# Kernel tuning notes

Measured on AMD Instinct MI355X. Metric: run time of the kernel, lower is better.

The kernel has to match this reference:

```python
import jax, jax.numpy as jnp
import numpy as np
import math

D_MODEL = 1024
N_HEADS = 16
D_K = D_MODEL // N_HEADS
SEQ_LEN = 2048
BATCH = 2


def setup_inputs() -> dict:
    key = jax.random.key(0)
    ks = jax.random.split(key, 5)
    X = jax.random.normal(ks[0], (BATCH, SEQ_LEN, D_MODEL), dtype=jnp.float32)
    # Linear params (torch Linear: y = x @ W.T + b). Store as [in, out] for einsum.
    sc1 = 1.0 / math.sqrt(D_MODEL)
    W_qkv = jax.random.uniform(ks[1], (D_MODEL, 3 * D_MODEL), jnp.float32, -sc1, sc1)
    b_qkv = jax.random.uniform(ks[2], (3 * D_MODEL,), jnp.float32, -sc1, sc1)
    W_out = jax.random.uniform(ks[3], (D_MODEL, D_MODEL), jnp.float32, -sc1, sc1)
    b_out = jax.random.uniform(ks[4], (D_MODEL,), jnp.float32, -sc1, sc1)
    return {"X": X, "W_qkv": W_qkv, "b_qkv": b_qkv, "W_out": W_out, "b_out": b_out}


def reference(X, W_qkv, b_qkv, W_out, b_out):
    B, S, E = X.shape
    qkv = X @ W_qkv + b_qkv                       # [B,S,3E]
    qkv = qkv.reshape(B, S, 3, N_HEADS, D_K)
    q = jnp.transpose(qkv[:, :, 0], (0, 2, 1, 3))  # [B,H,S,Dk]
    k = jnp.transpose(qkv[:, :, 1], (0, 2, 1, 3))
    v = jnp.transpose(qkv[:, :, 2], (0, 2, 1, 3))
    scores = jnp.einsum('bhqd,bhkd->bhqk', q, k) / math.sqrt(D_K)
    causal = jnp.tril(jnp.ones((S, S), dtype=bool))
    scores = jnp.where(causal[None, None], scores, -jnp.inf)
    probs = jax.nn.softmax(scores, axis=-1)
    out = jnp.einsum('bhqk,bhkd->bhqd', probs, v)  # [B,H,S,Dk]
    out = jnp.transpose(out, (0, 2, 1, 3)).reshape(B, S, E)
    return out @ W_out + b_out
```

## Files before the change

### kernel.cpp

```cpp
#include <hip/hip_runtime.h>

typedef __bf16 bf16_t;
typedef bf16_t bf16x8 __attribute__((ext_vector_type(8)));
typedef bf16_t bf16x4 __attribute__((ext_vector_type(4)));
typedef float f32x4 __attribute__((ext_vector_type(4)));

#define SEQLEN 2048
#define EMB 1024
#define NHEADS 16
#define N3 3072
#define NBATCH 2
#define NEG_INF (-__builtin_inff())
#define SC2 0.18033688011112042f

__device__ __forceinline__ void async16(bf16_t* lds, const bf16_t* g) {
    __builtin_amdgcn_global_load_lds(
        (const __attribute__((address_space(1))) void*)g,
        (__attribute__((address_space(3))) void*)lds, 16, 0, 0);
}

__global__ __launch_bounds__(256) void prep_kernel(
    const float* __restrict__ X, const float* __restrict__ Wqkv,
    const float* __restrict__ Wout, bf16_t* __restrict__ Xb,
    bf16_t* __restrict__ Wqkv_t, bf16_t* __restrict__ Wout_t)
{
    __shared__ float tile[64][65];
    const int id = blockIdx.x;
    const int t = threadIdx.x;
    if (id < 2048) {
        const int i = (id * 256 + t) * 8;
        float4 a = *(const float4*)&X[i];
        float4 b = *(const float4*)&X[i + 4];
        bf16_t v[8];
        v[0] = (bf16_t)a.x; v[1] = (bf16_t)a.y; v[2] = (bf16_t)a.z; v[3] = (bf16_t)a.w;
        v[4] = (bf16_t)b.x; v[5] = (bf16_t)b.y; v[6] = (bf16_t)b.z; v[7] = (bf16_t)b.w;
        *(float4*)&Xb[i] = *(float4*)&v[0];
        return;
    }
    const int wid2 = id - 2048;
    int bx = wid2 & 63;
    const int k0 = (wid2 >> 6) << 6;
    const float* W; bf16_t* Wt; int N; float s;
    if (bx < 48) { W = Wqkv; Wt = Wqkv_t; N = N3;  s = (bx * 64 < EMB) ? SC2 : 1.0f; }
    else         { bx -= 48; W = Wout; Wt = Wout_t; N = EMB; s = 1.0f; }
    const int n0 = bx * 64;
    const int nl = t & 63, k4 = t >> 6;
#pragma unroll
    for (int i = 0; i < 16; ++i) {
        int kk = k4 + i * 4;
        tile[kk][nl] = W[(size_t)(k0 + kk) * N + n0 + nl];
    }
    __syncthreads();
    const int kl = t & 63, n4 = t >> 6;
#pragma unroll
    for (int i = 0; i < 16; ++i) {
        int nn = n4 + i * 4;
        Wt[(size_t)(n0 + nn) * EMB + k0 + kl] = (bf16_t)(tile[kl][nn] * s);
    }
}

template<bool OUT_BF16, bool V_SPLIT>
__global__ __launch_bounds__(256) void gemm_bt_kernel(
    const bf16_t* __restrict__ A, const bf16_t* __restrict__ Bt,
    const float* __restrict__ bias, void* __restrict__ Cp,
    bf16_t* __restrict__ vt, int scale_q,
    int Mdim, int Ndim, int Kdim)
{
    __shared__ bf16_t As[128 * 64];
    __shared__ bf16_t Bs[128 * 64];
    const int nb = Ndim >> 7;
    const int cpx = gridDim.x >> 3;
    const int bid = (blockIdx.x & 7) * cpx + (blockIdx.x >> 3);
    const int bx = bid % nb, by = bid / nb;
    const int r0 = by << 7, c0 = bx << 7;
    const int t = threadIdx.x, lane = t & 63;
    const int wid = t >> 6;
    const int wm = wid >> 1, wn = wid & 1;
    const int lr = lane & 15, lg = lane >> 4;

    const int glrow = wid * 32 + (lane >> 3);
    const int gsw = ((lane & 7) ^ (lane >> 3)) << 3;
    const bf16_t* gA = &A[(size_t)(r0 + glrow) * Kdim + gsw];
    const bf16_t* gB = &Bt[(size_t)(c0 + glrow) * Kdim + gsw];
    bf16_t* ldsA = &As[wid * 2048];
    bf16_t* ldsB = &Bs[wid * 2048];
    const size_t row8 = (size_t)8 * Kdim;

    const int fragb0 = (lr * 128 + lg * 16) ^ ((lr & 7) << 4);
    const int fragb1 = (lr * 128 + 64 + lg * 16) ^ ((lr & 7) << 4);

    f32x4 acc[4][4] = {};
    const int KT = Kdim >> 6;
    for (int kt = 0; kt < KT; ++kt) {
        const bf16_t* a = gA + kt * 64;
        const bf16_t* b = gB + kt * 64;
        async16(ldsA,        a);
        async16(ldsA + 512,  a + row8);
        async16(ldsA + 1024, a + 2 * row8);
        async16(ldsA + 1536, a + 3 * row8);
        async16(ldsB,        b);
        async16(ldsB + 512,  b + row8);
        async16(ldsB + 1024, b + 2 * row8);
        async16(ldsB + 1536, b + 3 * row8);
        __syncthreads();

        const char* Ab = (const char*)As + wm * 8192;
        const char* Bb = (const char*)Bs + wn * 8192;
        bf16x8 af[4], bfm[4];
#pragma unroll
        for (int m = 0; m < 4; ++m)
            af[m] = *(const bf16x8*)(Ab + m * 2048 + fragb0);
#pragma unroll
        for (int n = 0; n < 4; ++n)
            bfm[n] = *(const bf16x8*)(Bb + n * 2048 + fragb0);
#pragma unroll
        for (int m = 0; m < 4; ++m)
#pragma unroll
            for (int n = 0; n < 4; ++n)
                acc[m][n] = __builtin_amdgcn_mfma_f32_16x16x32_bf16(
                    af[m], bfm[n], acc[m][n], 0, 0, 0);
#pragma unroll
        for (int m = 0; m < 4; ++m)
            af[m] = *(const bf16x8*)(Ab + m * 2048 + fragb1);
#pragma unroll
        for (int n = 0; n < 4; ++n)
            bfm[n] = *(const bf16x8*)(Bb + n * 2048 + fragb1);
#pragma unroll
        for (int m = 0; m < 4; ++m)
#pragma unroll
            for (int n = 0; n < 4; ++n)
                acc[m][n] = __builtin_amdgcn_mfma_f32_16x16x32_bf16(
                    af[m], bfm[n], acc[m][n], 0, 0, 0);
        __syncthreads();
    }

    const bool vmode = V_SPLIT && (c0 >= 2 * EMB);
    const int lgp = ((lg & 1) << 1) | (lg >> 1);
#pragma unroll
    for (int m = 0; m < 4; ++m) {
#pragma unroll
        for (int n = 0; n < 4; ++n) {
            const int col = c0 + wn * 64 + n * 16 + lr;
            float bval = bias[col];
            if (scale_q && col < EMB) bval *= SC2;
            if (vmode) {
                const int h = (col - 2 * EMB) >> 6, dd = col & 63;
                const int bb = r0 >> 11;
                const int sbase = (r0 & (SEQLEN - 1)) + wm * 64 + m * 16 + lgp * 4;
                bf16x4 pk;
#pragma unroll
                for (int j = 0; j < 4; ++j) pk[j] = (bf16_t)(acc[m][n][j] + bval);
                *(bf16x4*)&vt[(size_t)((bb * 16 + h) * 64 + dd) * SEQLEN + sbase] = pk;
            } else {
#pragma unroll
                for (int j = 0; j < 4; ++j) {
                    const int row = r0 + wm * 64 + m * 16 + lg * 4 + j;
                    const float v = acc[m][n][j] + bval;
                    if (OUT_BF16)
                        ((bf16_t*)Cp)[(size_t)row * Ndim + col] = (bf16_t)v;
                    else
                        ((float*)Cp)[(size_t)row * Ndim + col] = v;
                }
            }
        }
    }
}

__global__ __launch_bounds__(256, 4) void attn_kernel(
    const bf16_t* __restrict__ qkv, const bf16_t* __restrict__ vt,
    bf16_t* __restrict__ attn_out)
{
    __shared__ bf16_t Kl[2][4096];
    __shared__ bf16_t Vl[2][4096];
    const int d = blockIdx.x;
    const int r = d >> 8;
    const int u = (d >> 3) & 31;
    int qt = (r & 1) ? (31 - u) : u;
    if (r & 2) qt ^= 16;
    const int bh = (d & 7) + (r << 3);
    const int b = bh >> 4, h = bh & 15;
    const int q0 = qt << 6;
    const int t = threadIdx.x, lane = t & 63, wid = t >> 6;
    const int lr = lane & 15, lg = lane >> 4;
    const int sr = t >> 2, sc16 = (t & 3) << 4;

    const int fragb0 = (lr * 128 + lg * 16) ^ ((lr & 7) << 4);
    const int fragb1 = (lr * 128 + 64 + lg * 16) ^ ((lr & 7) << 4);
    const int stb0   = (sr * 128 + sc16 * 2) ^ ((sr & 7) << 4);
    const int stb1   = (sr * 128 + sc16 * 2 + 16) ^ ((sr & 7) << 4);

    const bf16_t* kp = &qkv[(size_t)(b * SEQLEN + sr) * N3 + EMB + h * 64 + sc16];
    const bf16_t* vp = &vt[(size_t)(bh * 64 + sr) * SEQLEN + sc16];
    const size_t kstep = (size_t)64 * N3;

    const int qg = q0 + wid * 16 + lr;
    bf16x8 qa0, qa1;
    {
        const bf16_t* qb = &qkv[(size_t)(b * SEQLEN + qg) * N3 + h * 64];
        qa0 = *(const bf16x8*)&qb[lg * 8];
        qa1 = *(const bf16x8*)&qb[32 + lg * 8];
    }
    bf16x8 ones;
#pragma unroll
    for (int i = 0; i < 8; ++i) ones[i] = (bf16_t)1.0f;

    f32x4 o[4] = {};
    f32x4 ol = {};
    float m_run = NEG_INF;

    auto stT = [&](char* base, float4 a, float4 c) {
        *(float4*)(base + stb0) = a; *(float4*)(base + stb1) = c;
    };

    {
        float4 k0 = *(const float4*)kp, k1 = *(const float4*)(kp + 8);
        float4 v0 = *(const float4*)vp, v1 = *(const float4*)(vp + 8);
        stT((char*)Kl[0], k0, k1);
        stT((char*)Vl[0], v0, v1);
    }
    __syncthreads();
    int cur = 0;
    for (int kt = 0; kt <= qt; ++kt) {
        float4 nk0, nk1, nv0, nv1;
        const bool more = (kt < qt);
        if (more) {
            kp += kstep; vp += 64;
            nk0 = *(const float4*)kp; nk1 = *(const float4*)(kp + 8);
            nv0 = *(const float4*)vp; nv1 = *(const float4*)(vp + 8);
        }

        const char* Kc = (const char*)Kl[cur];
        const char* Vc = (const char*)Vl[cur];

        f32x4 sc[4] = {};
        __builtin_amdgcn_s_setprio(1);
#pragma unroll
        for (int n = 0; n < 4; ++n) {
            bf16x8 kb0 = *(const bf16x8*)(Kc + (fragb0 + n * 2048));
            bf16x8 kb1 = *(const bf16x8*)(Kc + (fragb1 + n * 2048));
            sc[n] = __builtin_amdgcn_mfma_f32_16x16x32_bf16(kb0, qa0, sc[n], 0, 0, 0);
            sc[n] = __builtin_amdgcn_mfma_f32_16x16x32_bf16(kb1, qa1, sc[n], 0, 0, 0);
        }
        __builtin_amdgcn_s_setprio(0);

        if (kt == qt) {
#pragma unroll
            for (int n = 0; n < 4; ++n)
#pragma unroll
                for (int j = 0; j < 4; ++j) {
                    const int kg = kt * 64 + n * 16 + lg * 4 + j;
                    sc[n][j] = (kg <= qg) ? sc[n][j] : NEG_INF;
                }
        }
        float mx[4];
#pragma unroll
        for (int n = 0; n < 4; ++n)
            mx[n] = fmaxf(fmaxf(fmaxf(sc[n][0], sc[n][1]), sc[n][2]), sc[n][3]);
        float pmax = fmaxf(fmaxf(fmaxf(mx[0], mx[1]), mx[2]), mx[3]);

        if (__any(pmax > m_run + 8.f)) {
            float pm = fmaxf(pmax, __shfl_xor(pmax, 16));
            pm = fmaxf(pm, __shfl_xor(pm, 32));
            const float mnew = fmaxf(m_run, pm);
            const float alpha = exp2f(m_run - mnew);
            m_run = mnew;
            float al[4];
#pragma unroll
            for (int j = 0; j < 4; ++j) al[j] = __shfl(alpha, lg * 4 + j);
#pragma unroll
            for (int dn = 0; dn < 4; ++dn)
#pragma unroll
                for (int j = 0; j < 4; ++j) o[dn][j] *= al[j];
#pragma unroll
            for (int j = 0; j < 4; ++j) ol[j] *= al[j];
        }

#pragma unroll
        for (int n = 0; n < 4; ++n)
#pragma unroll
            for (int j = 0; j < 4; ++j) sc[n][j] = exp2f(sc[n][j] - m_run);

        unsigned pk00, pk01, pk10, pk11, pk20, pk21, pk30, pk31;
        asm("v_cvt_pk_bf16_f32 %0, %1, %2" : "=v"(pk00) : "v"(sc[0][0]), "v"(sc[0][1]));
        asm("v_cvt_pk_bf16_f32 %0, %1, %2" : "=v"(pk01) : "v"(sc[0][2]), "v"(sc[0][3]));
        asm("v_cvt_pk_bf16_f32 %0, %1, %2" : "=v"(pk10) : "v"(sc[1][0]), "v"(sc[1][1]));
        asm("v_cvt_pk_bf16_f32 %0, %1, %2" : "=v"(pk11) : "v"(sc[1][2]), "v"(sc[1][3]));
        asm("v_cvt_pk_bf16_f32 %0, %1, %2" : "=v"(pk20) : "v"(sc[2][0]), "v"(sc[2][1]));
        asm("v_cvt_pk_bf16_f32 %0, %1, %2" : "=v"(pk21) : "v"(sc[2][2]), "v"(sc[2][3]));
        asm("v_cvt_pk_bf16_f32 %0, %1, %2" : "=v"(pk30) : "v"(sc[3][0]), "v"(sc[3][1]));
        asm("v_cvt_pk_bf16_f32 %0, %1, %2" : "=v"(pk31) : "v"(sc[3][2]), "v"(sc[3][3]));
        asm("v_permlane32_swap_b32 %0, %1" : "+v"(pk00), "+v"(pk10));
        asm("v_permlane32_swap_b32 %0, %1" : "+v"(pk01), "+v"(pk11));
        asm("v_permlane32_swap_b32 %0, %1" : "+v"(pk20), "+v"(pk30));
        asm("v_permlane32_swap_b32 %0, %1" : "+v"(pk21), "+v"(pk31));
        union UW { unsigned w[4]; bf16x8 v; };
        UW ua, ub;
        ua.w[0] = pk00; ua.w[1] = pk01; ua.w[2] = pk10; ua.w[3] = pk11;
        ub.w[0] = pk20; ub.w[1] = pk21; ub.w[2] = pk30; ub.w[3] = pk31;
        const bf16x8 pa0 = ua.v, pa1 = ub.v;

        __builtin_amdgcn_s_setprio(1);
#pragma unroll
        for (int dn = 0; dn < 4; ++dn) {
            bf16x8 vb0 = *(const bf16x8*)(Vc + (fragb0 + dn * 2048));
            bf16x8 vb1 = *(const bf16x8*)(Vc + (fragb1 + dn * 2048));
            o[dn] = __builtin_amdgcn_mfma_f32_16x16x32_bf16(pa0, vb0, o[dn], 0, 0, 0);
            o[dn] = __builtin_amdgcn_mfma_f32_16x16x32_bf16(pa1, vb1, o[dn], 0, 0, 0);
        }
        ol = __builtin_amdgcn_mfma_f32_16x16x32_bf16(pa0, ones, ol, 0, 0, 0);
        ol = __builtin_amdgcn_mfma_f32_16x16x32_bf16(pa1, ones, ol, 0, 0, 0);
        __builtin_amdgcn_s_setprio(0);

        if (more) {
            stT((char*)Kl[cur ^ 1], nk0, nk1);
            stT((char*)Vl[cur ^ 1], nv0, nv1);
        }
        __syncthreads();
        cur ^= 1;
    }

    float li[4];
#pragma unroll
    for (int j = 0; j < 4; ++j) li[j] = 1.0f / ol[j];
#pragma unroll
    for (int dn = 0; dn < 4; ++dn)
#pragma unroll
        for (int j = 0; j < 4; ++j) {
            const int row = b * SEQLEN + q0 + wid * 16 + lg * 4 + j;
            attn_out[(size_t)row * EMB + h * 64 + dn * 16 + lr] =
                (bf16_t)(o[dn][j] * li[j]);
        }
}

extern "C" void kernel_launch(void* const* d_in, const int* in_sizes, int n_in,
                              void* d_out, int out_size, void* d_ws, size_t ws_size,
                              hipStream_t stream)
{
    const float* X     = (const float*)d_in[0];
    const float* W_qkv = (const float*)d_in[1];
    const float* b_qkv = (const float*)d_in[2];
    const float* W_out = (const float*)d_in[3];
    const float* b_out = (const float*)d_in[4];
    float* out = (float*)d_out;

    char* ws = (char*)d_ws;
    bf16_t* Wqkv_t = (bf16_t*)ws;
    bf16_t* Wout_t = (bf16_t*)(ws + 6u * 1024 * 1024);
    bf16_t* qkv    = (bf16_t*)(ws + 8u * 1024 * 1024);
    bf16_t* attn   = (bf16_t*)(ws + 32u * 1024 * 1024);
    bf16_t* Xb     = (bf16_t*)(ws + 40u * 1024 * 1024);
    bf16_t* Vt_g   = (bf16_t*)(ws + 48u * 1024 * 1024);

    dim3 blk(256);
    prep_kernel<<<3072, blk, 0, stream>>>(X, W_qkv, W_out, Xb, Wqkv_t, Wout_t);

    gemm_bt_kernel<true, true><<<(4096 / 128) * (N3 / 128), blk, 0, stream>>>(
        Xb, Wqkv_t, b_qkv, (void*)qkv, Vt_g, 1, 4096, N3, EMB);

    attn_kernel<<<32 * 32, blk, 0, stream>>>(qkv, Vt_g, attn);

    gemm_bt_kernel<false, false><<<(4096 / 128) * (EMB / 128), blk, 0, stream>>>(
        attn, Wout_t, b_out, (void*)out, nullptr, 0, 4096, EMB, EMB);
}
```

Before: 108.3 us.

## Use 128-row query tiles with 8 waves sharing each K/V tile in attention

The attention kernel now launches 512 blocks of 512 threads, each covering 128 query rows, so eight waves share one staged K/V tile instead of four. Each thread loads one 16-byte chunk per tile, and waves whose queries lie entirely before a key tile skip its compute while still joining the barrier. The block-to-tile mapping is changed to pair long and short causal tiles. This halves K/V global loads and LDS staging per query, at the cost of idle waves on diagonal tiles and fewer, larger blocks.

```diff
diff --git a/kernel.cpp b/kernel.cpp
--- a/kernel.cpp
+++ b/kernel.cpp
@@ -166,7 +166,7 @@
     }
 }
 
-__global__ __launch_bounds__(256, 4) void attn_kernel(
+__global__ __launch_bounds__(512, 4) void attn_kernel(
     const bf16_t* __restrict__ qkv, const bf16_t* __restrict__ vt,
     bf16_t* __restrict__ attn_out)
 {
@@ -174,31 +174,31 @@
     __shared__ bf16_t Vl[2][4096];
     const int d = blockIdx.x;
     const int r = d >> 8;
-    const int u = (d >> 3) & 31;
-    int qt = (r & 1) ? (31 - u) : u;
-    if (r & 2) qt ^= 16;
-    const int bh = (d & 7) + (r << 3);
+    const int u = (d >> 5) & 7;
+    const int bh = d & 31;
+    const int qt = r ? u : (15 - u);
     const int b = bh >> 4, h = bh & 15;
-    const int q0 = qt << 6;
+    const int q0 = qt << 7;
+    const int ktend = 2 * qt + 1;
     const int t = threadIdx.x, lane = t & 63, wid = t >> 6;
     const int lr = lane & 15, lg = lane >> 4;
-    const int sr = t >> 2, sc16 = (t & 3) << 4;
+    const int sr = t >> 3, sc8 = (t & 7) << 3;
 
     const int fragb0 = (lr * 128 + lg * 16) ^ ((lr & 7) << 4);
     const int fragb1 = (lr * 128 + 64 + lg * 16) ^ ((lr & 7) << 4);
-    const int stb0   = (sr * 128 + sc16 * 2) ^ ((sr & 7) << 4);
-    const int stb1   = (sr * 128 + sc16 * 2 + 16) ^ ((sr & 7) << 4);
-
-    const bf16_t* kp = &qkv[(size_t)(b * SEQLEN + sr) * N3 + EMB + h * 64 + sc16];
-    const bf16_t* vp = &vt[(size_t)(bh * 64 + sr) * SEQLEN + sc16];
+    const int stb    = (sr * 128 + sc8 * 2) ^ ((sr & 7) << 4);
+
+    const bf16_t* kp = &qkv[(size_t)(b * SEQLEN + sr) * N3 + EMB + h * 64 + sc8];
+    const bf16_t* vp = &vt[(size_t)(bh * 64 + sr) * SEQLEN + sc8];
     const size_t kstep = (size_t)64 * N3;
 
-    const int qg = q0 + wid * 16 + lr;
+    const int qb = q0 + wid * 16;
+    const int qg = qb + lr;
     bf16x8 qa0, qa1;
     {
-        const bf16_t* qb = &qkv[(size_t)(b * SEQLEN + qg) * N3 + h * 64];
-        qa0 = *(const bf16x8*)&qb[lg * 8];
-        qa1 = *(const bf16x8*)&qb[32 + lg * 8];
+        const bf16_t* qp = &qkv[(size_t)(b * SEQLEN + qg) * N3 + h * 64];
+        qa0 = *(const bf16x8*)&qp[lg * 8];
+        qa1 = *(const bf16x8*)&qp[32 + lg * 8];
     }
     bf16x8 ones;
 #pragma unroll
@@ -208,112 +208,111 @@
     f32x4 ol = {};
     float m_run = NEG_INF;
 
-    auto stT = [&](char* base, float4 a, float4 c) {
-        *(float4*)(base + stb0) = a; *(float4*)(base + stb1) = c;
-    };
-
     {
-        float4 k0 = *(const float4*)kp, k1 = *(const float4*)(kp + 8);
-        float4 v0 = *(const float4*)vp, v1 = *(const float4*)(vp + 8);
-        stT((char*)Kl[0], k0, k1);
-        stT((char*)Vl[0], v0, v1);
+        float4 k0 = *(const float4*)kp;
+        float4 v0 = *(const float4*)vp;
+        *(float4*)((char*)Kl[0] + stb) = k0;
+        *(float4*)((char*)Vl[0] + stb) = v0;
     }
     __syncthreads();
     int cur = 0;
-    for (int kt = 0; kt <= qt; ++kt) {
-        float4 nk0, nk1, nv0, nv1;
-        const bool more = (kt < qt);
+    for (int kt = 0; kt <= ktend; ++kt) {
+        float4 nk, nv;
+        const bool more = (kt < ktend);
         if (more) {
             kp += kstep; vp += 64;
-            nk0 = *(const float4*)kp; nk1 = *(const float4*)(kp + 8);
-            nv0 = *(const float4*)vp; nv1 = *(const float4*)(vp + 8);
-        }
-
-        const char* Kc = (const char*)Kl[cur];
-        const char* Vc = (const char*)Vl[cur];
-
-        f32x4 sc[4] = {};
-        __builtin_amdgcn_s_setprio(1);
-#pragma unroll
-        for (int n = 0; n < 4; ++n) {
-            bf16x8 kb0 = *(const bf16x8*)(Kc + (fragb0 + n * 2048));
-            bf16x8 kb1 = *(const bf16x8*)(Kc + (fragb1 + n * 2048));
-            sc[n] = __builtin_amdgcn_mfma_f32_16x16x32_bf16(kb0, qa0, sc[n], 0, 0, 0);
-            sc[n] = __builtin_amdgcn_mfma_f32_16x16x32_bf16(kb1, qa1, sc[n], 0, 0, 0);
-        }
-        __builtin_amdgcn_s_setprio(0);
-
-        if (kt == qt) {
+            nk = *(const float4*)kp;
+            nv = *(const float4*)vp;
+        }
+
+        const int kbase = kt << 6;
+        if (kbase <= qb + 15) {
+            const char* Kc = (const char*)Kl[cur];
+            const char* Vc = (const char*)Vl[cur];
+
+            f32x4 sc[4] = {};
+            __builtin_amdgcn_s_setprio(1);
+#pragma unroll
+            for (int n = 0; n < 4; ++n) {
+                bf16x8 kb0 = *(const bf16x8*)(Kc + (fragb0 + n * 2048));
+                bf16x8 kb1 = *(const bf16x8*)(Kc + (fragb1 + n * 2048));
+                sc[n] = __builtin_amdgcn_mfma_f32_16x16x32_bf16(kb0, qa0, sc[n], 0, 0, 0);
+                sc[n] = __builtin_amdgcn_mfma_f32_16x16x32_bf16(kb1, qa1, sc[n], 0, 0, 0);
+            }
+            __builtin_amdgcn_s_setprio(0);
+
+            if (kbase + 63 > qb) {
+#pragma unroll
+                for (int n = 0; n < 4; ++n)
+#pragma unroll
+                    for (int j = 0; j < 4; ++j) {
+                        const int kg = kbase + n * 16 + lg * 4 + j;
+                        sc[n][j] = (kg <= qg) ? sc[n][j] : NEG_INF;
+                    }
+            }
+            float mx[4];
 #pragma unroll
             for (int n = 0; n < 4; ++n)
-#pragma unroll
-                for (int j = 0; j < 4; ++j) {
-                    const int kg = kt * 64 + n * 16 + lg * 4 + j;
-                    sc[n][j] = (kg <= qg) ? sc[n][j] : NEG_INF;
-                }
-        }
-        float mx[4];
-#pragma unroll
-        for (int n = 0; n < 4; ++n)
-            mx[n] = fmaxf(fmaxf(fmaxf(sc[n][0], sc[n][1]), sc[n][2]), sc[n][3]);
-        float pmax = fmaxf(fmaxf(fmaxf(mx[0], mx[1]), mx[2]), mx[3]);
-
-        if (__any(pmax > m_run + 8.f)) {
-            float pm = fmaxf(pmax, __shfl_xor(pmax, 16));
-            pm = fmaxf(pm, __shfl_xor(pm, 32));
-            const float mnew = fmaxf(m_run, pm);
-            const float alpha = exp2f(m_run - mnew);
-            m_run = mnew;
-            float al[4];
-#pragma unroll
-            for (int j = 0; j < 4; ++j) al[j] = __shfl(alpha, lg * 4 + j);
-#pragma unroll
-            for (int dn = 0; dn < 4; ++dn)
-#pragma unroll
-                for (int j = 0; j < 4; ++j) o[dn][j] *= al[j];
-#pragma unroll
-            for (int j = 0; j < 4; ++j) ol[j] *= al[j];
-        }
-
-#pragma unroll
-        for (int n = 0; n < 4; ++n)
-#pragma unroll
-            for (int j = 0; j < 4; ++j) sc[n][j] = exp2f(sc[n][j] - m_run);
-
-        unsigned pk00, pk01, pk10, pk11, pk20, pk21, pk30, pk31;
-        asm("v_cvt_pk_bf16_f32 %0, %1, %2" : "=v"(pk00) : "v"(sc[0][0]), "v"(sc[0][1]));
-        asm("v_cvt_pk_bf16_f32 %0, %1, %2" : "=v"(pk01) : "v"(sc[0][2]), "v"(sc[0][3]));
-        asm("v_cvt_pk_bf16_f32 %0, %1, %2" : "=v"(pk10) : "v"(sc[1][0]), "v"(sc[1][1]));
-        asm("v_cvt_pk_bf16_f32 %0, %1, %2" : "=v"(pk11) : "v"(sc[1][2]), "v"(sc[1][3]));
-        asm("v_cvt_pk_bf16_f32 %0, %1, %2" : "=v"(pk20) : "v"(sc[2][0]), "v"(sc[2][1]));
-        asm("v_cvt_pk_bf16_f32 %0, %1, %2" : "=v"(pk21) : "v"(sc[2][2]), "v"(sc[2][3]));
-        asm("v_cvt_pk_bf16_f32 %0, %1, %2" : "=v"(pk30) : "v"(sc[3][0]), "v"(sc[3][1]));
-        asm("v_cvt_pk_bf16_f32 %0, %1, %2" : "=v"(pk31) : "v"(sc[3][2]), "v"(sc[3][3]));
-        asm("v_permlane32_swap_b32 %0, %1" : "+v"(pk00), "+v"(pk10));
-        asm("v_permlane32_swap_b32 %0, %1" : "+v"(pk01), "+v"(pk11));
-        asm("v_permlane32_swap_b32 %0, %1" : "+v"(pk20), "+v"(pk30));
-        asm("v_permlane32_swap_b32 %0, %1" : "+v"(pk21), "+v"(pk31));
-        union UW { unsigned w[4]; bf16x8 v; };
-        UW ua, ub;
-        ua.w[0] = pk00; ua.w[1] = pk01; ua.w[2] = pk10; ua.w[3] = pk11;
-        ub.w[0] = pk20; ub.w[1] = pk21; ub.w[2] = pk30; ub.w[3] = pk31;
-        const bf16x8 pa0 = ua.v, pa1 = ub.v;
-
-        __builtin_amdgcn_s_setprio(1);
-#pragma unroll
-        for (int dn = 0; dn < 4; ++dn) {
-            bf16x8 vb0 = *(const bf16x8*)(Vc + (fragb0 + dn * 2048));
-            bf16x8 vb1 = *(const bf16x8*)(Vc + (fragb1 + dn * 2048));
-            o[dn] = __builtin_amdgcn_mfma_f32_16x16x32_bf16(pa0, vb0, o[dn], 0, 0, 0);
-            o[dn] = __builtin_amdgcn_mfma_f32_16x16x32_bf16(pa1, vb1, o[dn], 0, 0, 0);
-        }
-        ol = __builtin_amdgcn_mfma_f32_16x16x32_bf16(pa0, ones, ol, 0, 0, 0);
-        ol = __builtin_amdgcn_mfma_f32_16x16x32_bf16(pa1, ones, ol, 0, 0, 0);
-        __builtin_amdgcn_s_setprio(0);
+                mx[n] = fmaxf(fmaxf(fmaxf(sc[n][0], sc[n][1]), sc[n][2]), sc[n][3]);
+            float pmax = fmaxf(fmaxf(fmaxf(mx[0], mx[1]), mx[2]), mx[3]);
+
+            if (__any(pmax > m_run + 8.f)) {
+                float pm = fmaxf(pmax, __shfl_xor(pmax, 16));
+                pm = fmaxf(pm, __shfl_xor(pm, 32));
+                const float mnew = fmaxf(m_run, pm);
+                const float alpha = exp2f(m_run - mnew);
+                m_run = mnew;
+                float al[4];
+#pragma unroll
+                for (int j = 0; j < 4; ++j) al[j] = __shfl(alpha, lg * 4 + j);
+#pragma unroll
+                for (int dn = 0; dn < 4; ++dn)
+#pragma unroll
+                    for (int j = 0; j < 4; ++j) o[dn][j] *= al[j];
+#pragma unroll
+                for (int j = 0; j < 4; ++j) ol[j] *= al[j];
+            }
+
+#pragma unroll
+            for (int n = 0; n < 4; ++n)
+#pragma unroll
+                for (int j = 0; j < 4; ++j) sc[n][j] = exp2f(sc[n][j] - m_run);
+
+            unsigned pk00, pk01, pk10, pk11, pk20, pk21, pk30, pk31;
+            asm("v_cvt_pk_bf16_f32 %0, %1, %2" : "=v"(pk00) : "v"(sc[0][0]), "v"(sc[0][1]));
+            asm("v_cvt_pk_bf16_f32 %0, %1, %2" : "=v"(pk01) : "v"(sc[0][2]), "v"(sc[0][3]));
+            asm("v_cvt_pk_bf16_f32 %0, %1, %2" : "=v"(pk10) : "v"(sc[1][0]), "v"(sc[1][1]));
+            asm("v_cvt_pk_bf16_f32 %0, %1, %2" : "=v"(pk11) : "v"(sc[1][2]), "v"(sc[1][3]));
+            asm("v_cvt_pk_bf16_f32 %0, %1, %2" : "=v"(pk20) : "v"(sc[2][0]), "v"(sc[2][1]));
+            asm("v_cvt_pk_bf16_f32 %0, %1, %2" : "=v"(pk21) : "v"(sc[2][2]), "v"(sc[2][3]));
+            asm("v_cvt_pk_bf16_f32 %0, %1, %2" : "=v"(pk30) : "v"(sc[3][0]), "v"(sc[3][1]));
+            asm("v_cvt_pk_bf16_f32 %0, %1, %2" : "=v"(pk31) : "v"(sc[3][2]), "v"(sc[3][3]));
+            asm("v_permlane32_swap_b32 %0, %1" : "+v"(pk00), "+v"(pk10));
+            asm("v_permlane32_swap_b32 %0, %1" : "+v"(pk01), "+v"(pk11));
+            asm("v_permlane32_swap_b32 %0, %1" : "+v"(pk20), "+v"(pk30));
+            asm("v_permlane32_swap_b32 %0, %1" : "+v"(pk21), "+v"(pk31));
+            union UW { unsigned w[4]; bf16x8 v; };
+            UW ua, ub;
+            ua.w[0] = pk00; ua.w[1] = pk01; ua.w[2] = pk10; ua.w[3] = pk11;
+            ub.w[0] = pk20; ub.w[1] = pk21; ub.w[2] = pk30; ub.w[3] = pk31;
+            const bf16x8 pa0 = ua.v, pa1 = ub.v;
+
+            __builtin_amdgcn_s_setprio(1);
+#pragma unroll
+            for (int dn = 0; dn < 4; ++dn) {
+                bf16x8 vb0 = *(const bf16x8*)(Vc + (fragb0 + dn * 2048));
+                bf16x8 vb1 = *(const bf16x8*)(Vc + (fragb1 + dn * 2048));
+                o[dn] = __builtin_amdgcn_mfma_f32_16x16x32_bf16(pa0, vb0, o[dn], 0, 0, 0);
+                o[dn] = __builtin_amdgcn_mfma_f32_16x16x32_bf16(pa1, vb1, o[dn], 0, 0, 0);
+            }
+            ol = __builtin_amdgcn_mfma_f32_16x16x32_bf16(pa0, ones, ol, 0, 0, 0);
+            ol = __builtin_amdgcn_mfma_f32_16x16x32_bf16(pa1, ones, ol, 0, 0, 0);
+            __builtin_amdgcn_s_setprio(0);
+        }
 
         if (more) {
-            stT((char*)Kl[cur ^ 1], nk0, nk1);
-            stT((char*)Vl[cur ^ 1], nv0, nv1);
+            *(float4*)((char*)Kl[cur ^ 1] + stb) = nk;
+            *(float4*)((char*)Vl[cur ^ 1] + stb) = nv;
         }
         __syncthreads();
         cur ^= 1;
@@ -326,7 +325,7 @@
     for (int dn = 0; dn < 4; ++dn)
 #pragma unroll
         for (int j = 0; j < 4; ++j) {
-            const int row = b * SEQLEN + q0 + wid * 16 + lg * 4 + j;
+            const int row = b * SEQLEN + qb + lg * 4 + j;
             attn_out[(size_t)row * EMB + h * 64 + dn * 16 + lr] =
                 (bf16_t)(o[dn][j] * li[j]);
         }
@@ -357,7 +356,7 @@
     gemm_bt_kernel<true, true><<<(4096 / 128) * (N3 / 128), blk, 0, stream>>>(
         Xb, Wqkv_t, b_qkv, (void*)qkv, Vt_g, 1, 4096, N3, EMB);
 
-    attn_kernel<<<32 * 32, blk, 0, stream>>>(qkv, Vt_g, attn);
+    attn_kernel<<<512, dim3(512), 0, stream>>>(qkv, Vt_g, attn);
 
     gemm_bt_kernel<false, false><<<(4096 / 128) * (EMB / 128), blk, 0, stream>>>(
         attn, Wout_t, b_out, (void*)out, nullptr, 0, 4096, EMB, EMB);
```

Measured after the change: 106.6 us. No clear change (-1.6%).
